# Optimization experiments

Measured on AMD Instinct MI355X. Metric: run time of the kernel, lower is better.

Reference implementation:

```python
import jax, jax.numpy as jnp
import numpy as np

NEG_SLOPE = 0.2  # PyG GATConv default negative_slope
H1, H2, H3 = 4, 4, 1
CH = 64  # hidden_dim (per-head out channels)
N_NODES = 50000
N_EDGES = 800000
IN_DIM = 128
N_CLASSES = 10


def _gat_layer(x, src, dst, n, W, a_src, a_dst, b, heads, ch):
    # x: [N, Fin], W: [Fin, heads*ch], a_src/a_dst: [heads, ch], b: [heads*ch]
    h = (x @ W).reshape(-1, heads, ch)              # [N, H, C]
    e_src = jnp.sum(h * a_src, axis=-1)             # [N, H]
    e_dst = jnp.sum(h * a_dst, axis=-1)             # [N, H]
    e = jax.nn.leaky_relu(e_src[src] + e_dst[dst], NEG_SLOPE)  # [E, H]
    # segment softmax over incoming edges of each dst node
    m = jax.ops.segment_max(e, dst, num_segments=n)            # [N, H]
    p = jnp.exp(e - m[dst])                                    # [E, H]
    s = jax.ops.segment_sum(p, dst, num_segments=n)            # [N, H]
    alpha = p / (s[dst] + 1e-16)                               # [E, H]
    out = jax.ops.segment_sum(alpha[:, :, None] * h[src], dst, num_segments=n)  # [N, H, C]
    return out.reshape(-1, heads * ch) + b


def setup_inputs() -> dict:
    key = jax.random.key(0)
    ks = jax.random.split(key, 16)

    def glorot(k, shape, fan_in):
        return jax.random.normal(k, shape, dtype=jnp.float32) * (1.0 / np.sqrt(fan_in))

    x = jax.random.normal(ks[0], (N_NODES, IN_DIM), dtype=jnp.float32)
    edge_index = jax.random.randint(ks[1], (2, N_EDGES), 0, N_NODES, dtype=jnp.int32)

    d1 = H1 * CH  # 256
    d2 = H2 * CH  # 256
    d3 = H3 * CH  # 64
    return {
        "x": x,
        "edge_index": edge_index,
        "W1": glorot(ks[2], (IN_DIM, d1), IN_DIM),
        "a1_src": glorot(ks[3], (H1, CH), CH),
        "a1_dst": glorot(ks[4], (H1, CH), CH),
        "b1": jnp.zeros((d1,), jnp.float32),
        "W2": glorot(ks[5], (d1, d2), d1),
        "a2_src": glorot(ks[6], (H2, CH), CH),
        "a2_dst": glorot(ks[7], (H2, CH), CH),
        "b2": jnp.zeros((d2,), jnp.float32),
        "W3": glorot(ks[8], (d2, d3), d2),
        "a3_src": glorot(ks[9], (H3, CH), CH),
        "a3_dst": glorot(ks[10], (H3, CH), CH),
        "b3": jnp.zeros((d3,), jnp.float32),
        "fc_W": glorot(ks[11], (CH, N_CLASSES), CH),
        "fc_b": jnp.zeros((N_CLASSES,), jnp.float32),
    }


def reference(x, edge_index, W1, a1_src, a1_dst, b1, W2, a2_src, a2_dst, b2,
              W3, a3_src, a3_dst, b3, fc_W, fc_b):
    n = x.shape[0]
    # PyG GATConv adds self-loops by default
    loops = jnp.arange(n, dtype=edge_index.dtype)
    src = jnp.concatenate([edge_index[0], loops])
    dst = jnp.concatenate([edge_index[1], loops])

    h = jax.nn.relu(_gat_layer(x, src, dst, n, W1, a1_src, a1_dst, b1, H1, CH))
    # dropout(p=0.3) is identity in eval mode
    h = jax.nn.relu(_gat_layer(h, src, dst, n, W2, a2_src, a2_dst, b2, H2, CH))
    h = jax.nn.relu(_gat_layer(h, src, dst, n, W3, a3_src, a3_dst, b3, H3, CH))
    return h @ fc_W + fc_b  # [N, num_classes]
```

## Files before the change

kernel.cpp:

```cpp
#include <hip/hip_runtime.h>

#define NN 50000
#define NE 800000
#define E2 (NE + NN)
#define IN_DIM 128
#define SCAN_B 196

typedef unsigned short u16;
typedef unsigned int u32;
typedef __attribute__((ext_vector_type(8))) short short8;
typedef __attribute__((ext_vector_type(4))) float f32x4;

__device__ inline u16 f2bf(float x) {
    u32 u = __float_as_uint(x);
    u32 r = (u + 0x7fff + ((u >> 16) & 1)) >> 16;
    return (u16)r;
}
__device__ inline float bf2f(u16 h) { return __uint_as_float(((u32)h) << 16); }

__global__ __launch_bounds__(256) void fill_i32(int* __restrict__ p, int v, int n) {
    int i = blockIdx.x * 256 + threadIdx.x;
    if (i < n) p[i] = v;
}

__global__ __launch_bounds__(256) void hist_dst(const int* __restrict__ ei, int* __restrict__ deg) {
    int e = blockIdx.x * 256 + threadIdx.x;
    if (e < NE) atomicAdd(&deg[ei[NE + e]], 1);
}

__global__ __launch_bounds__(256) void block_sums(const int* __restrict__ deg, int* __restrict__ bsum) {
    int b = blockIdx.x;
    int i = b * 256 + threadIdx.x;
    int v = (i < NN) ? deg[i] : 0;
#pragma unroll
    for (int off = 32; off; off >>= 1) v += __shfl_down(v, off);
    __shared__ int ws[4];
    if ((threadIdx.x & 63) == 0) ws[threadIdx.x >> 6] = v;
    __syncthreads();
    if (threadIdx.x == 0) bsum[b] = ws[0] + ws[1] + ws[2] + ws[3];
}

__global__ __launch_bounds__(256) void scan_bsums(const int* __restrict__ bsum, int* __restrict__ boff) {
    __shared__ int s[256];
    int t = threadIdx.x;
    int v = (t < SCAN_B) ? bsum[t] : 0;
    s[t] = v;
    __syncthreads();
    for (int off = 1; off < 256; off <<= 1) {
        int u = (t >= off) ? s[t - off] : 0;
        __syncthreads();
        s[t] += u;
        __syncthreads();
    }
    if (t < SCAN_B) boff[t] = s[t] - v;
}

__global__ __launch_bounds__(256) void scan_final(const int* __restrict__ deg,
                                                  const int* __restrict__ boff,
                                                  int* __restrict__ rowptr,
                                                  int* __restrict__ cursor) {
    int b = blockIdx.x;
    int t = threadIdx.x;
    int i = b * 256 + t;
    int v = (i < NN) ? deg[i] : 0;
    __shared__ int s[256];
    s[t] = v;
    __syncthreads();
    for (int off = 1; off < 256; off <<= 1) {
        int u = (t >= off) ? s[t - off] : 0;
        __syncthreads();
        s[t] += u;
        __syncthreads();
    }
    int excl = s[t] - v + boff[b];
    if (i < NN) { rowptr[i] = excl; cursor[i] = excl; }
    if (i == NN - 1) rowptr[NN] = excl + v;
}

__global__ __launch_bounds__(256) void scatter_csr(const int* __restrict__ ei,
                                                   int* __restrict__ cursor,
                                                   int* __restrict__ csr_src) {
    int e = blockIdx.x * 256 + threadIdx.x;
    if (e >= E2) return;
    int s, d;
    if (e < NE) { s = ei[e]; d = ei[NE + e]; } else { s = d = e - NE; }
    int pos = atomicAdd(&cursor[d], 1);
    csr_src[pos] = s;
}

__global__ __launch_bounds__(256) void xconv(const float* __restrict__ X,
                                             u16* __restrict__ Xh, u16* __restrict__ Xl,
                                             int total4) {
    int i = blockIdx.x * 256 + threadIdx.x;
    if (i >= total4) return;
    float4 v = reinterpret_cast<const float4*>(X)[i];
    ushort4 h, l;
    h.x = f2bf(v.x); l.x = f2bf(v.x - bf2f(h.x));
    h.y = f2bf(v.y); l.y = f2bf(v.y - bf2f(h.y));
    h.z = f2bf(v.z); l.z = f2bf(v.z - bf2f(h.z));
    h.w = f2bf(v.w); l.w = f2bf(v.w - bf2f(h.w));
    reinterpret_cast<ushort4*>(Xh)[i] = h;
    reinterpret_cast<ushort4*>(Xl)[i] = l;
}

__global__ __launch_bounds__(256) void wconv(const float* __restrict__ W,
                                             u16* __restrict__ Wh, u16* __restrict__ Wl,
                                             int K, int N) {
    int idx = blockIdx.x * 256 + threadIdx.x;
    if (idx >= K * N) return;
    int k = idx / N, n = idx - k * N;
    float w = W[idx];
    u16 hi = f2bf(w);
    Wh[(size_t)n * K + k] = hi;
    Wl[(size_t)n * K + k] = f2bf(w - bf2f(hi));
}

template<int BN, int KK, bool FES>
__global__ __launch_bounds__(256) void gemm_mfma(const u16* __restrict__ Ah,
                                                 const u16* __restrict__ Al,
                                                 const u16* __restrict__ Wh,
                                                 const u16* __restrict__ Wl,
                                                 float* __restrict__ C,
                                                 int M, int N,
                                                 const float* __restrict__ as_,
                                                 const float* __restrict__ ad_,
                                                 float* __restrict__ es,
                                                 float* __restrict__ ed) {
    const int BM = 128, BK = 32, LDT = BK + 8;
    __shared__ u16 Ahs[2][BM][LDT], Als[2][BM][LDT];
    const int FRN = BN / 32;
    int tid = threadIdx.x;
    int lane = tid & 63, wid = tid >> 6;
    int wm = wid >> 1, wn = wid & 1;
    int row0 = blockIdx.x * BM, col0 = blockIdx.y * BN;
    int l15 = lane & 15, lg = lane >> 4;

    int c0 = tid * 2;
    int r_a = c0 >> 2, sub_a0 = (c0 & 3) * 8, sub_a1 = ((c0 + 1) & 3) * 8;
    int gr_a = row0 + r_a;

    uint4 avh[2], avl[2];
    auto loadA = [&](int ko) {
        if (gr_a < M) {
            avh[0] = *reinterpret_cast<const uint4*>(Ah + (size_t)gr_a * KK + ko + sub_a0);
            avl[0] = *reinterpret_cast<const uint4*>(Al + (size_t)gr_a * KK + ko + sub_a0);
            avh[1] = *reinterpret_cast<const uint4*>(Ah + (size_t)gr_a * KK + ko + sub_a1);
            avl[1] = *reinterpret_cast<const uint4*>(Al + (size_t)gr_a * KK + ko + sub_a1);
        } else {
            avh[0] = avh[1] = avl[0] = avl[1] = make_uint4(0, 0, 0, 0);
        }
    };
    auto writeA = [&](int p) {
        *reinterpret_cast<uint4*>(&Ahs[p][r_a][sub_a0]) = avh[0];
        *reinterpret_cast<uint4*>(&Als[p][r_a][sub_a0]) = avl[0];
        *reinterpret_cast<uint4*>(&Ahs[p][r_a][sub_a1]) = avh[1];
        *reinterpret_cast<uint4*>(&Als[p][r_a][sub_a1]) = avl[1];
    };

    f32x4 acc[4][FRN];
#pragma unroll
    for (int i = 0; i < 4; ++i)
#pragma unroll
        for (int j = 0; j < FRN; ++j) acc[i][j] = (f32x4){0.f, 0.f, 0.f, 0.f};

    loadA(0);
    writeA(0);
    loadA(BK);
    __syncthreads();

    for (int ko = 0; ko < KK; ko += BK) {
        int p = (ko >> 5) & 1;
        if (ko + BK < KK) {
            writeA(p ^ 1);
            if (ko + 2 * BK < KK) loadA(ko + 2 * BK);
        }
        short8 bh[FRN], bl[FRN];
#pragma unroll
        for (int j = 0; j < FRN; ++j) {
            int gc = col0 + wn * (BN / 2) + j * 16 + l15;
            bh[j] = *reinterpret_cast<const short8*>(Wh + (size_t)gc * KK + ko + lg * 8);
            bl[j] = *reinterpret_cast<const short8*>(Wl + (size_t)gc * KK + ko + lg * 8);
        }
        short8 ah[4], al[4];
#pragma unroll
        for (int i = 0; i < 4; ++i) {
            int r = wm * 64 + i * 16 + l15;
            ah[i] = *reinterpret_cast<const short8*>(&Ahs[p][r][lg * 8]);
            al[i] = *reinterpret_cast<const short8*>(&Als[p][r][lg * 8]);
        }
#pragma unroll
        for (int i = 0; i < 4; ++i)
#pragma unroll
            for (int j = 0; j < FRN; ++j) {
                acc[i][j] = __builtin_amdgcn_mfma_f32_16x16x32_bf16(ah[i], bh[j], acc[i][j], 0, 0, 0);
                acc[i][j] = __builtin_amdgcn_mfma_f32_16x16x32_bf16(ah[i], bl[j], acc[i][j], 0, 0, 0);
                acc[i][j] = __builtin_amdgcn_mfma_f32_16x16x32_bf16(al[i], bh[j], acc[i][j], 0, 0, 0);
            }
        __syncthreads();
    }
#pragma unroll
    for (int i = 0; i < 4; ++i)
#pragma unroll
        for (int rr = 0; rr < 4; ++rr) {
            int gr = row0 + wm * 64 + i * 16 + lg * 4 + rr;
            if (gr < M) {
#pragma unroll
                for (int j = 0; j < FRN; ++j)
                    C[(size_t)gr * N + col0 + wn * (BN / 2) + j * 16 + l15] = acc[i][j][rr];
            }
        }
    if (FES) {
        int head = (col0 + wn * (BN / 2)) >> 6;
        float asv[FRN], adv[FRN];
#pragma unroll
        for (int j = 0; j < FRN; ++j) {
            asv[j] = as_[head * 64 + j * 16 + l15];
            adv[j] = ad_[head * 64 + j * 16 + l15];
        }
#pragma unroll
        for (int i = 0; i < 4; ++i)
#pragma unroll
            for (int rr = 0; rr < 4; ++rr) {
                float vs = 0.f, vd = 0.f;
#pragma unroll
                for (int j = 0; j < FRN; ++j) {
                    vs += acc[i][j][rr] * asv[j];
                    vd += acc[i][j][rr] * adv[j];
                }
#pragma unroll
                for (int off = 1; off < 16; off <<= 1) {
                    vs += __shfl_xor(vs, off);
                    vd += __shfl_xor(vd, off);
                }
                int gr = row0 + wm * 64 + i * 16 + lg * 4 + rr;
                if (l15 == 0 && gr < M) {
                    es[gr * 4 + head] = vs;
                    ed[gr * 4 + head] = vd;
                }
            }
    }
}

__global__ void escore(const float* __restrict__ h, const float* __restrict__ as,
                       const float* __restrict__ ad, float* __restrict__ es,
                       float* __restrict__ ed, int H) {
    int n = blockIdx.x;
    int t = threadIdx.x;
    int D = blockDim.x;
    float hv = h[(size_t)n * D + t];
    float vs = hv * as[t];
    float vd = hv * ad[t];
#pragma unroll
    for (int off = 32; off; off >>= 1) {
        vs += __shfl_down(vs, off);
        vd += __shfl_down(vd, off);
    }
    if ((t & 63) == 0) {
        int head = t >> 6;
        es[n * H + head] = vs;
        ed[n * H + head] = vd;
    }
}

template<int D, int H, bool FC>
__global__ __launch_bounds__(256) void agg_fused(const int* __restrict__ rowptr,
                                                 const int* __restrict__ csr_src,
                                                 const float* __restrict__ es,
                                                 const float* __restrict__ ed,
                                                 const float* __restrict__ h,
                                                 const float* __restrict__ b,
                                                 u16* __restrict__ Oh,
                                                 u16* __restrict__ Ol,
                                                 const float* __restrict__ fcW,
                                                 const float* __restrict__ fcb,
                                                 float* __restrict__ out) {
    const int TPN = D / 4;
    const int NPB = 256 / TPN;
    const int logH = (H == 4) ? 2 : 0;
    int tid = threadIdx.x;
    int n = blockIdx.x * NPB + tid / TPN;
    if (n >= NN) return;
    int gl = tid % TPN;
    int start = rowptr[n], end = rowptr[n + 1];

    int headA = gl & (H - 1);
    const int JP = TPN >> logH;
    float edvA = ed[n * H + headA];
    float m = -1e30f;
    for (int i = start + (gl >> logH); i < end; i += JP) {
        int src = csr_src[i];
        float v = es[src * H + headA] + edvA;
        v = v > 0.f ? v : 0.2f * v;
        m = fmaxf(m, v);
    }
#pragma unroll
    for (int off = H; off < TPN; off <<= 1)
        m = fmaxf(m, __shfl_xor(m, off));

    int f0 = gl * 4;
    int hb = f0 >> 6;
    float mB;
    if (D == 256) mB = __shfl(m, hb);
    else          mB = m;
    float edv = ed[n * H + hb];
    float sump = 0.f;
    float4 acc = make_float4(0.f, 0.f, 0.f, 0.f);
    int i = start;
    for (; i + 8 <= end; i += 8) {
        int s0 = csr_src[i + 0], s1 = csr_src[i + 1], s2 = csr_src[i + 2], s3 = csr_src[i + 3];
        int s4 = csr_src[i + 4], s5 = csr_src[i + 5], s6 = csr_src[i + 6], s7 = csr_src[i + 7];
        float v0 = es[s0 * H + hb] + edv, v1 = es[s1 * H + hb] + edv;
        float v2 = es[s2 * H + hb] + edv, v3 = es[s3 * H + hb] + edv;
        float v4 = es[s4 * H + hb] + edv, v5 = es[s5 * H + hb] + edv;
        float v6 = es[s6 * H + hb] + edv, v7 = es[s7 * H + hb] + edv;
        v0 = v0 > 0.f ? v0 : 0.2f * v0; v1 = v1 > 0.f ? v1 : 0.2f * v1;
        v2 = v2 > 0.f ? v2 : 0.2f * v2; v3 = v3 > 0.f ? v3 : 0.2f * v3;
        v4 = v4 > 0.f ? v4 : 0.2f * v4; v5 = v5 > 0.f ? v5 : 0.2f * v5;
        v6 = v6 > 0.f ? v6 : 0.2f * v6; v7 = v7 > 0.f ? v7 : 0.2f * v7;
        float p0 = __expf(v0 - mB), p1 = __expf(v1 - mB);
        float p2 = __expf(v2 - mB), p3 = __expf(v3 - mB);
        float p4 = __expf(v4 - mB), p5 = __expf(v5 - mB);
        float p6 = __expf(v6 - mB), p7 = __expf(v7 - mB);
        float4 h0 = *reinterpret_cast<const float4*>(h + (size_t)s0 * D + f0);
        float4 h1 = *reinterpret_cast<const float4*>(h + (size_t)s1 * D + f0);
        float4 h2 = *reinterpret_cast<const float4*>(h + (size_t)s2 * D + f0);
        float4 h3 = *reinterpret_cast<const float4*>(h + (size_t)s3 * D + f0);
        float4 h4 = *reinterpret_cast<const float4*>(h + (size_t)s4 * D + f0);
        float4 h5 = *reinterpret_cast<const float4*>(h + (size_t)s5 * D + f0);
        float4 h6 = *reinterpret_cast<const float4*>(h + (size_t)s6 * D + f0);
        float4 h7 = *reinterpret_cast<const float4*>(h + (size_t)s7 * D + f0);
        acc.x += p0 * h0.x + p1 * h1.x + p2 * h2.x + p3 * h3.x
               + p4 * h4.x + p5 * h5.x + p6 * h6.x + p7 * h7.x;
        acc.y += p0 * h0.y + p1 * h1.y + p2 * h2.y + p3 * h3.y
               + p4 * h4.y + p5 * h5.y + p6 * h6.y + p7 * h7.y;
        acc.z += p0 * h0.z + p1 * h1.z + p2 * h2.z + p3 * h3.z
               + p4 * h4.z + p5 * h5.z + p6 * h6.z + p7 * h7.z;
        acc.w += p0 * h0.w + p1 * h1.w + p2 * h2.w + p3 * h3.w
               + p4 * h4.w + p5 * h5.w + p6 * h6.w + p7 * h7.w;
        sump += p0 + p1 + p2 + p3 + p4 + p5 + p6 + p7;
    }
    for (; i < end; ++i) {
        int s0 = csr_src[i];
        float v = es[s0 * H + hb] + edv;
        v = v > 0.f ? v : 0.2f * v;
        float p = __expf(v - mB);
        float4 h0 = *reinterpret_cast<const float4*>(h + (size_t)s0 * D + f0);
        acc.x += p * h0.x; acc.y += p * h0.y; acc.z += p * h0.z; acc.w += p * h0.w;
        sump += p;
    }
    float inv = 1.f / (sump + 1e-16f);
    float4 bb = *reinterpret_cast<const float4*>(b + f0);
    float4 o;
    o.x = acc.x * inv + bb.x; o.y = acc.y * inv + bb.y;
    o.z = acc.z * inv + bb.z; o.w = acc.w * inv + bb.w;
    o.x = o.x > 0.f ? o.x : 0.f; o.y = o.y > 0.f ? o.y : 0.f;
    o.z = o.z > 0.f ? o.z : 0.f; o.w = o.w > 0.f ? o.w : 0.f;
    if (!FC) {
        ushort4 hv, lv;
        hv.x = f2bf(o.x); lv.x = f2bf(o.x - bf2f(hv.x));
        hv.y = f2bf(o.y); lv.y = f2bf(o.y - bf2f(hv.y));
        hv.z = f2bf(o.z); lv.z = f2bf(o.z - bf2f(hv.z));
        hv.w = f2bf(o.w); lv.w = f2bf(o.w - bf2f(hv.w));
        *reinterpret_cast<ushort4*>(Oh + (size_t)n * D + f0) = hv;
        *reinterpret_cast<ushort4*>(Ol + (size_t)n * D + f0) = lv;
    } else {
        float pj[10];
#pragma unroll
        for (int j = 0; j < 10; ++j)
            pj[j] = o.x * fcW[(f0 + 0) * 10 + j] + o.y * fcW[(f0 + 1) * 10 + j]
                  + o.z * fcW[(f0 + 2) * 10 + j] + o.w * fcW[(f0 + 3) * 10 + j];
#pragma unroll
        for (int off = 1; off < 16; off <<= 1)
#pragma unroll
            for (int j = 0; j < 10; ++j)
                pj[j] += __shfl_xor(pj[j], off);
        if (gl < 10)
            out[n * 10 + gl] = pj[0] * 0.f + (gl == 0 ? 0.f : 0.f) + pj[gl] + fcb[gl];
    }
}


extern "C" void kernel_launch(void* const* d_in, const int* in_sizes, int n_in,
                              void* d_out, int out_size, void* d_ws, size_t ws_size,
                              hipStream_t stream) {
    const float* x   = (const float*)d_in[0];
    const int*   ei  = (const int*)d_in[1];
    const float* W1  = (const float*)d_in[2];
    const float* a1s = (const float*)d_in[3];
    const float* a1d = (const float*)d_in[4];
    const float* b1  = (const float*)d_in[5];
    const float* W2  = (const float*)d_in[6];
    const float* a2s = (const float*)d_in[7];
    const float* a2d = (const float*)d_in[8];
    const float* b2  = (const float*)d_in[9];
    const float* W3  = (const float*)d_in[10];
    const float* a3s = (const float*)d_in[11];
    const float* a3d = (const float*)d_in[12];
    const float* b3  = (const float*)d_in[13];
    const float* fcW = (const float*)d_in[14];
    const float* fcb = (const float*)d_in[15];
    float* out = (float*)d_out;

    char* wp = (char*)d_ws;
    float* h   = (float*)wp;  wp += (size_t)NN * 256 * 4;
    u16* Ph    = (u16*)wp;    wp += (size_t)NN * 256 * 2;
    u16* Pl    = (u16*)wp;    wp += (size_t)NN * 256 * 2;
    u16* Xh    = (u16*)wp;    wp += (size_t)NN * 128 * 2;
    u16* Xl    = (u16*)wp;    wp += (size_t)NN * 128 * 2;
    float* ES  = (float*)wp;  wp += (size_t)NN * 4 * 4;
    float* ED  = (float*)wp;  wp += (size_t)NN * 4 * 4;
    u16* Wth   = (u16*)wp;    wp += 256 * 256 * 2;
    u16* Wtl   = (u16*)wp;    wp += 256 * 256 * 2;
    int* rowptr = (int*)wp;   wp += (NN + 1) * 4;
    int* csrsrc = (int*)wp;   wp += (size_t)E2 * 4;
    int* deg    = (int*)wp;   wp += NN * 4;
    int* bsum   = (int*)wp;   wp += 256 * 4;
    int* boff   = (int*)wp;   wp += 256 * 4;
    int* cursor = (int*)((char*)d_ws + (size_t)NN * 256 * 4);

    fill_i32<<<(NN + 255) / 256, 256, 0, stream>>>(deg, 1, NN);
    hist_dst<<<(NE + 255) / 256, 256, 0, stream>>>(ei, deg);
    block_sums<<<SCAN_B, 256, 0, stream>>>(deg, bsum);
    scan_bsums<<<1, 256, 0, stream>>>(bsum, boff);
    scan_final<<<SCAN_B, 256, 0, stream>>>(deg, boff, rowptr, cursor);
    scatter_csr<<<(E2 + 255) / 256, 256, 0, stream>>>(ei, cursor, csrsrc);

    xconv<<<(NN * IN_DIM / 4 + 255) / 256, 256, 0, stream>>>(x, Xh, Xl, NN * IN_DIM / 4);

    const int MT = (NN + 127) / 128;

    wconv<<<(IN_DIM * 256 + 255) / 256, 256, 0, stream>>>(W1, Wth, Wtl, IN_DIM, 256);
    gemm_mfma<128, 128, true><<<dim3(MT, 2), 256, 0, stream>>>(Xh, Xl, Wth, Wtl, h, NN, 256,
                                                               a1s, a1d, ES, ED);
    agg_fused<256, 4, false><<<(NN + 3) / 4, 256, 0, stream>>>(rowptr, csrsrc, ES, ED, h, b1,
                                                               Ph, Pl, nullptr, nullptr, nullptr);

    wconv<<<(256 * 256 + 255) / 256, 256, 0, stream>>>(W2, Wth, Wtl, 256, 256);
    gemm_mfma<128, 256, true><<<dim3(MT, 2), 256, 0, stream>>>(Ph, Pl, Wth, Wtl, h, NN, 256,
                                                               a2s, a2d, ES, ED);
    agg_fused<256, 4, false><<<(NN + 3) / 4, 256, 0, stream>>>(rowptr, csrsrc, ES, ED, h, b2,
                                                               Ph, Pl, nullptr, nullptr, nullptr);

    wconv<<<(256 * 64 + 255) / 256, 256, 0, stream>>>(W3, Wth, Wtl, 256, 64);
    gemm_mfma<64, 256, false><<<dim3(MT, 1), 256, 0, stream>>>(Ph, Pl, Wth, Wtl, h, NN, 64,
                                                               nullptr, nullptr, nullptr, nullptr);
    escore<<<NN, 64, 0, stream>>>(h, a3s, a3d, ES, ED, 1);
    agg_fused<64, 1, true><<<(NN + 15) / 16, 256, 0, stream>>>(rowptr, csrsrc, ES, ED, h, b3,
                                                               nullptr, nullptr, fcW, fcb, out);
}
```

Measured before the change: 529.6 us.

## Fuse layer-3 score computation into GEMM and software-pipeline edge aggregation loads

Removes the separate escore kernel for layer 3 by computing the attention scores in the GEMM epilogue. For BN=64 the two wave-column halves are reduced through shared memory. The aggregation loop is double-buffered so gathers for the next 8 edges are issued before the current 8 are consumed, which hides gather latency at the cost of more registers. The FC output selection is also rewritten to avoid dynamic register indexing.

```diff
diff --git a/kernel.cpp b/kernel.cpp
--- a/kernel.cpp
+++ b/kernel.cpp
@@ -210,57 +210,104 @@
             }
         }
     if (FES) {
-        int head = (col0 + wn * (BN / 2)) >> 6;
-        float asv[FRN], adv[FRN];
-#pragma unroll
-        for (int j = 0; j < FRN; ++j) {
-            asv[j] = as_[head * 64 + j * 16 + l15];
-            adv[j] = ad_[head * 64 + j * 16 + l15];
-        }
-#pragma unroll
-        for (int i = 0; i < 4; ++i)
-#pragma unroll
-            for (int rr = 0; rr < 4; ++rr) {
-                float vs = 0.f, vd = 0.f;
-#pragma unroll
-                for (int j = 0; j < FRN; ++j) {
-                    vs += acc[i][j][rr] * asv[j];
-                    vd += acc[i][j][rr] * adv[j];
+        if constexpr (BN == 128) {
+            int head = (col0 + wn * (BN / 2)) >> 6;
+            float asv[FRN], adv[FRN];
+#pragma unroll
+            for (int j = 0; j < FRN; ++j) {
+                asv[j] = as_[head * 64 + j * 16 + l15];
+                adv[j] = ad_[head * 64 + j * 16 + l15];
+            }
+#pragma unroll
+            for (int i = 0; i < 4; ++i)
+#pragma unroll
+                for (int rr = 0; rr < 4; ++rr) {
+                    float vs = 0.f, vd = 0.f;
+#pragma unroll
+                    for (int j = 0; j < FRN; ++j) {
+                        vs += acc[i][j][rr] * asv[j];
+                        vd += acc[i][j][rr] * adv[j];
+                    }
+#pragma unroll
+                    for (int off = 1; off < 16; off <<= 1) {
+                        vs += __shfl_xor(vs, off);
+                        vd += __shfl_xor(vd, off);
+                    }
+                    int gr = row0 + wm * 64 + i * 16 + lg * 4 + rr;
+                    if (l15 == 0 && gr < M) {
+                        es[gr * 4 + head] = vs;
+                        ed[gr * 4 + head] = vd;
+                    }
                 }
-#pragma unroll
-                for (int off = 1; off < 16; off <<= 1) {
-                    vs += __shfl_xor(vs, off);
-                    vd += __shfl_xor(vd, off);
+        } else {
+            __shared__ float esp[2][BM], edp[2][BM];
+            float asv[FRN], adv[FRN];
+#pragma unroll
+            for (int j = 0; j < FRN; ++j) {
+                asv[j] = as_[wn * (BN / 2) + j * 16 + l15];
+                adv[j] = ad_[wn * (BN / 2) + j * 16 + l15];
+            }
+#pragma unroll
+            for (int i = 0; i < 4; ++i)
+#pragma unroll
+                for (int rr = 0; rr < 4; ++rr) {
+                    float vs = 0.f, vd = 0.f;
+#pragma unroll
+                    for (int j = 0; j < FRN; ++j) {
+                        vs += acc[i][j][rr] * asv[j];
+                        vd += acc[i][j][rr] * adv[j];
+                    }
+#pragma unroll
+                    for (int off = 1; off < 16; off <<= 1) {
+                        vs += __shfl_xor(vs, off);
+                        vd += __shfl_xor(vd, off);
+                    }
+                    int rl = wm * 64 + i * 16 + lg * 4 + rr;
+                    if (l15 == 0) { esp[wn][rl] = vs; edp[wn][rl] = vd; }
                 }
-                int gr = row0 + wm * 64 + i * 16 + lg * 4 + rr;
-                if (l15 == 0 && gr < M) {
-                    es[gr * 4 + head] = vs;
-                    ed[gr * 4 + head] = vd;
+            __syncthreads();
+            if (tid < BM) {
+                int gr = row0 + tid;
+                if (gr < M) {
+                    es[gr] = esp[0][tid] + esp[1][tid];
+                    ed[gr] = edp[0][tid] + edp[1][tid];
                 }
             }
-    }
-}
-
-__global__ void escore(const float* __restrict__ h, const float* __restrict__ as,
-                       const float* __restrict__ ad, float* __restrict__ es,
-                       float* __restrict__ ed, int H) {
-    int n = blockIdx.x;
-    int t = threadIdx.x;
-    int D = blockDim.x;
-    float hv = h[(size_t)n * D + t];
-    float vs = hv * as[t];
-    float vd = hv * ad[t];
-#pragma unroll
-    for (int off = 32; off; off >>= 1) {
-        vs += __shfl_down(vs, off);
-        vd += __shfl_down(vd, off);
-    }
-    if ((t & 63) == 0) {
-        int head = t >> 6;
-        es[n * H + head] = vs;
-        ed[n * H + head] = vd;
-    }
-}
+        }
+    }
+}
+
+#define LOADC(S, E, HF, base)                                                     \
+    {                                                                             \
+        S##0 = csr_src[(base) + 0]; S##1 = csr_src[(base) + 1];                   \
+        S##2 = csr_src[(base) + 2]; S##3 = csr_src[(base) + 3];                   \
+        S##4 = csr_src[(base) + 4]; S##5 = csr_src[(base) + 5];                   \
+        S##6 = csr_src[(base) + 6]; S##7 = csr_src[(base) + 7];                   \
+        E##0 = es[S##0 * H + hb]; E##1 = es[S##1 * H + hb];                       \
+        E##2 = es[S##2 * H + hb]; E##3 = es[S##3 * H + hb];                       \
+        E##4 = es[S##4 * H + hb]; E##5 = es[S##5 * H + hb];                       \
+        E##6 = es[S##6 * H + hb]; E##7 = es[S##7 * H + hb];                       \
+        HF##0 = *reinterpret_cast<const float4*>(h + (size_t)S##0 * D + f0);      \
+        HF##1 = *reinterpret_cast<const float4*>(h + (size_t)S##1 * D + f0);      \
+        HF##2 = *reinterpret_cast<const float4*>(h + (size_t)S##2 * D + f0);      \
+        HF##3 = *reinterpret_cast<const float4*>(h + (size_t)S##3 * D + f0);      \
+        HF##4 = *reinterpret_cast<const float4*>(h + (size_t)S##4 * D + f0);      \
+        HF##5 = *reinterpret_cast<const float4*>(h + (size_t)S##5 * D + f0);      \
+        HF##6 = *reinterpret_cast<const float4*>(h + (size_t)S##6 * D + f0);      \
+        HF##7 = *reinterpret_cast<const float4*>(h + (size_t)S##7 * D + f0);      \
+    }
+#define CONS1(Eq, HFq)                                                            \
+    {                                                                             \
+        float v = Eq + edv;                                                       \
+        v = v > 0.f ? v : 0.2f * v;                                               \
+        float p = __expf(v - mB);                                                 \
+        acc.x += p * HFq.x; acc.y += p * HFq.y;                                   \
+        acc.z += p * HFq.z; acc.w += p * HFq.w;                                   \
+        sump += p;                                                                \
+    }
+#define CONSC(E, HF)                                                              \
+    CONS1(E##0, HF##0) CONS1(E##1, HF##1) CONS1(E##2, HF##2) CONS1(E##3, HF##3)   \
+    CONS1(E##4, HF##4) CONS1(E##5, HF##5) CONS1(E##6, HF##6) CONS1(E##7, HF##7)
 
 template<int D, int H, bool FC>
 __global__ __launch_bounds__(256) void agg_fused(const int* __restrict__ rowptr,
@@ -305,49 +352,42 @@
     float edv = ed[n * H + hb];
     float sump = 0.f;
     float4 acc = make_float4(0.f, 0.f, 0.f, 0.f);
+
+    int sA0, sA1, sA2, sA3, sA4, sA5, sA6, sA7;
+    int sB0, sB1, sB2, sB3, sB4, sB5, sB6, sB7;
+    float eA0, eA1, eA2, eA3, eA4, eA5, eA6, eA7;
+    float eB0, eB1, eB2, eB3, eB4, eB5, eB6, eB7;
+    float4 hA0, hA1, hA2, hA3, hA4, hA5, hA6, hA7;
+    float4 hB0, hB1, hB2, hB3, hB4, hB5, hB6, hB7;
+
     int i = start;
-    for (; i + 8 <= end; i += 8) {
-        int s0 = csr_src[i + 0], s1 = csr_src[i + 1], s2 = csr_src[i + 2], s3 = csr_src[i + 3];
-        int s4 = csr_src[i + 4], s5 = csr_src[i + 5], s6 = csr_src[i + 6], s7 = csr_src[i + 7];
-        float v0 = es[s0 * H + hb] + edv, v1 = es[s1 * H + hb] + edv;
-        float v2 = es[s2 * H + hb] + edv, v3 = es[s3 * H + hb] + edv;
-        float v4 = es[s4 * H + hb] + edv, v5 = es[s5 * H + hb] + edv;
-        float v6 = es[s6 * H + hb] + edv, v7 = es[s7 * H + hb] + edv;
-        v0 = v0 > 0.f ? v0 : 0.2f * v0; v1 = v1 > 0.f ? v1 : 0.2f * v1;
-        v2 = v2 > 0.f ? v2 : 0.2f * v2; v3 = v3 > 0.f ? v3 : 0.2f * v3;
-        v4 = v4 > 0.f ? v4 : 0.2f * v4; v5 = v5 > 0.f ? v5 : 0.2f * v5;
-        v6 = v6 > 0.f ? v6 : 0.2f * v6; v7 = v7 > 0.f ? v7 : 0.2f * v7;
-        float p0 = __expf(v0 - mB), p1 = __expf(v1 - mB);
-        float p2 = __expf(v2 - mB), p3 = __expf(v3 - mB);
-        float p4 = __expf(v4 - mB), p5 = __expf(v5 - mB);
-        float p6 = __expf(v6 - mB), p7 = __expf(v7 - mB);
-        float4 h0 = *reinterpret_cast<const float4*>(h + (size_t)s0 * D + f0);
-        float4 h1 = *reinterpret_cast<const float4*>(h + (size_t)s1 * D + f0);
-        float4 h2 = *reinterpret_cast<const float4*>(h + (size_t)s2 * D + f0);
-        float4 h3 = *reinterpret_cast<const float4*>(h + (size_t)s3 * D + f0);
-        float4 h4 = *reinterpret_cast<const float4*>(h + (size_t)s4 * D + f0);
-        float4 h5 = *reinterpret_cast<const float4*>(h + (size_t)s5 * D + f0);
-        float4 h6 = *reinterpret_cast<const float4*>(h + (size_t)s6 * D + f0);
-        float4 h7 = *reinterpret_cast<const float4*>(h + (size_t)s7 * D + f0);
-        acc.x += p0 * h0.x + p1 * h1.x + p2 * h2.x + p3 * h3.x
-               + p4 * h4.x + p5 * h5.x + p6 * h6.x + p7 * h7.x;
-        acc.y += p0 * h0.y + p1 * h1.y + p2 * h2.y + p3 * h3.y
-               + p4 * h4.y + p5 * h5.y + p6 * h6.y + p7 * h7.y;
-        acc.z += p0 * h0.z + p1 * h1.z + p2 * h2.z + p3 * h3.z
-               + p4 * h4.z + p5 * h5.z + p6 * h6.z + p7 * h7.z;
-        acc.w += p0 * h0.w + p1 * h1.w + p2 * h2.w + p3 * h3.w
-               + p4 * h4.w + p5 * h5.w + p6 * h6.w + p7 * h7.w;
-        sump += p0 + p1 + p2 + p3 + p4 + p5 + p6 + p7;
+    int nf = (end - start) >> 3;
+    if (nf) {
+        LOADC(sA, eA, hA, i);
+        i += 8; --nf;
+        while (nf >= 2) {
+            LOADC(sB, eB, hB, i);
+            CONSC(eA, hA);
+            LOADC(sA, eA, hA, i + 8);
+            CONSC(eB, hB);
+            i += 16; nf -= 2;
+        }
+        if (nf) {
+            LOADC(sB, eB, hB, i);
+            CONSC(eA, hA);
+            CONSC(eB, hB);
+            i += 8;
+        } else {
+            CONSC(eA, hA);
+        }
     }
     for (; i < end; ++i) {
         int s0 = csr_src[i];
-        float v = es[s0 * H + hb] + edv;
-        v = v > 0.f ? v : 0.2f * v;
-        float p = __expf(v - mB);
+        float e0 = es[s0 * H + hb];
         float4 h0 = *reinterpret_cast<const float4*>(h + (size_t)s0 * D + f0);
-        acc.x += p * h0.x; acc.y += p * h0.y; acc.z += p * h0.z; acc.w += p * h0.w;
-        sump += p;
-    }
+        CONS1(e0, h0);
+    }
+
     float inv = 1.f / (sump + 1e-16f);
     float4 bb = *reinterpret_cast<const float4*>(b + f0);
     float4 o;
@@ -374,11 +414,14 @@
 #pragma unroll
             for (int j = 0; j < 10; ++j)
                 pj[j] += __shfl_xor(pj[j], off);
-        if (gl < 10)
-            out[n * 10 + gl] = pj[0] * 0.f + (gl == 0 ? 0.f : 0.f) + pj[gl] + fcb[gl];
-    }
-}
-
+        if (gl < 10) {
+            float r = 0.f;
+#pragma unroll
+            for (int j = 0; j < 10; ++j) if (gl == j) r = pj[j];
+            out[n * 10 + gl] = r + fcb[gl];
+        }
+    }
+}
 
 extern "C" void kernel_launch(void* const* d_in, const int* in_sizes, int n_in,
                               void* d_out, int out_size, void* d_ws, size_t ws_size,
@@ -442,9 +485,8 @@
                                                                Ph, Pl, nullptr, nullptr, nullptr);
 
     wconv<<<(256 * 64 + 255) / 256, 256, 0, stream>>>(W3, Wth, Wtl, 256, 64);
-    gemm_mfma<64, 256, false><<<dim3(MT, 1), 256, 0, stream>>>(Ph, Pl, Wth, Wtl, h, NN, 64,
-                                                               nullptr, nullptr, nullptr, nullptr);
-    escore<<<NN, 64, 0, stream>>>(h, a3s, a3d, ES, ED, 1);
+    gemm_mfma<64, 256, true><<<dim3(MT, 1), 256, 0, stream>>>(Ph, Pl, Wth, Wtl, h, NN, 64,
+                                                              a3s, a3d, ES, ED);
     agg_fused<64, 1, true><<<(NN + 15) / 16, 256, 0, stream>>>(rowptr, csrsrc, ES, ED, h, b3,
                                                                nullptr, nullptr, fcW, fcb, out);
 }
```

After: 533.8 us. No clear change (+0.8%).
